# Kernel optimization log

Hardware: AMD Instinct MI355X
Metric: run time of the kernel (lower is better)

The kernel has to match this reference:

```python
import math
import jax, jax.numpy as jnp
import numpy as np

H = 16  # num_heads
B, L, D = 1, 256, 1024


def setup_inputs() -> dict:
    key = jax.random.key(0)
    ks = jax.random.split(key, 12)
    s = 1.0 / math.sqrt(D)  # keep activations O(1)
    inp = {
        "mu": jax.random.normal(ks[0], (B, L, D), jnp.float32),
        "var": jax.random.uniform(ks[1], (B, L, D), jnp.float32) + 0.1,
    }
    names = ["q_mu", "q_var", "k_mu", "k_var", "v_mu", "v_var", "o_mu", "o_var"]
    for i, n in enumerate(names):
        inp["w" + n] = jax.random.normal(ks[2 + i], (D, D), jnp.float32) * s
        inp["b" + n] = jnp.zeros((D,), jnp.float32)
    return inp


def _split_heads(x):
    b, l, d = x.shape
    return x.reshape(b, l, H, d // H).transpose(0, 2, 1, 3)  # [B,H,L,Dh]


def _combine_heads(x):
    b, h, l, dh = x.shape
    return x.transpose(0, 2, 1, 3).reshape(b, l, h * dh)


def reference(mu, var, wq_mu, bq_mu, wq_var, bq_var, wk_mu, bk_mu, wk_var, bk_var,
              wv_mu, bv_mu, wv_var, bv_var, wo_mu, bo_mu, wo_var, bo_var):
    dk = mu.shape[-1] // H
    Qm = _split_heads(mu @ wq_mu + bq_mu)
    Qv = _split_heads(jax.nn.softplus(var @ wq_var + bq_var))
    Km = _split_heads(mu @ wk_mu + bk_mu)
    Kv = _split_heads(jax.nn.softplus(var @ wk_var + bk_var))
    Vm = _split_heads(mu @ wv_mu + bv_mu)
    Vv = _split_heads(jax.nn.softplus(var @ wv_var + bv_var))

    # per-element Gaussian KL, broadcast to [B,H,Lq,Lk,Dh] (as in the original)
    diff = (Qm[:, :, :, None, :] - Km[:, :, None, :, :]) ** 2
    ratio = Qv[:, :, :, None, :] / Kv[:, :, None, :, :]
    kl = diff / (2.0 * Kv[:, :, None, :, :]) + 0.5 * (ratio - jnp.log(ratio) - 1.0)
    scores = -kl.sum(-1) * (1.0 / math.sqrt(dk))  # [B,H,Lq,Lk]
    attn = jax.nn.softmax(scores, axis=-1)

    out_mu = jnp.einsum("bhqk,bhkd->bhqd", attn, Vm)
    out_var = jnp.einsum("bhqk,bhkd->bhqd", attn ** 2, Vv)

    O_mu = _combine_heads(out_mu)
    O_var = _combine_heads(out_var)
    mu_out = O_mu @ wo_mu + bo_mu
    var_out = jax.nn.softplus(O_var @ wo_var + bo_var)
    return mu_out, var_out
```

## Files before the change

kernel.cpp:

```cpp
#include <hip/hip_runtime.h>
#include <math.h>

typedef __bf16 bf16_t;
typedef bf16_t bf16x4 __attribute__((ext_vector_type(4)));
typedef bf16_t bf16x8 __attribute__((ext_vector_type(8)));
typedef float  f32x4  __attribute__((ext_vector_type(4)));

__device__ __forceinline__ float softplus_f(float x) {
    return (x > 20.f) ? x : log1pf(expf(x));
}

__device__ __forceinline__ float fast_rcp(float x) {
#if __has_builtin(__builtin_amdgcn_rcpf)
    return __builtin_amdgcn_rcpf(x);
#else
    return 1.0f / x;
#endif
}

template<bool AF32, int MT>
__device__ __forceinline__ void gemmT_core(const void* Aptr, const float* __restrict__ Wf,
                                           const int m_base, const int n_base,
                                           unsigned char* smem, const int t, f32x4* out) {
    constexpr int NA  = 2 * MT;
    constexpr int SWS = MT * 1152 + 4608;
    constexpr int CRS = MT * 1088;
    __syncthreads();
    bf16_t* stage = (bf16_t*)smem;
    float*  Cr    = (float*)smem;
    const int lane = t & 63, w = t >> 6;
    bf16_t* As = stage + w * SWS;
    bf16_t* Bs = As + MT * 1152;
    const int r8 = lane >> 3, kb = lane & 7;
    const int fr = lane & 15, fq = lane >> 4, fk = fq * 8;
    const int bc = fr;
    const int br16 = fq * 16;

    const float*  Af = (const float*)Aptr  + (size_t)m_base * 1024 + w * 256 + kb * 8;
    const bf16_t* Ab = (const bf16_t*)Aptr + (size_t)m_base * 1024 + w * 256 + kb * 8;
    const float*  Bf = Wf + (size_t)(w * 256 + br16) * 1024 + n_base + bc * 4;

    f32x4 acc[MT][4] = {};
    bf16x8 pa[NA];
    f32x4 paf0[NA], paf1[NA];
    f32x4 pbf[16];

#pragma unroll
    for (int i = 0; i < NA; ++i) {
        if constexpr (AF32) {
            paf0[i] = *(const f32x4*)(Af + (size_t)(i * 8 + r8) * 1024);
            paf1[i] = *(const f32x4*)(Af + (size_t)(i * 8 + r8) * 1024 + 4);
        } else {
            pa[i] = *(const bf16x8*)(Ab + (size_t)(i * 8 + r8) * 1024);
        }
    }
#pragma unroll
    for (int i = 0; i < 16; ++i)
        pbf[i] = *(const f32x4*)(Bf + (size_t)i * 1024);

#pragma unroll
    for (int s = 0; s < 4; ++s) {
#pragma unroll
        for (int i = 0; i < NA; ++i) {
            bf16x8 av;
            if constexpr (AF32) {
#pragma unroll
                for (int e = 0; e < 4; ++e) {
                    av[e]     = (bf16_t)paf0[i][e];
                    av[e + 4] = (bf16_t)paf1[i][e];
                }
            } else {
                av = pa[i];
            }
            *(bf16x8*)&As[(i * 8 + r8) * 72 + kb * 8] = av;
        }
#pragma unroll
        for (int e = 0; e < 4; ++e) {
            bf16x8 lo, hi;
#pragma unroll
            for (int q = 0; q < 8; ++q) {
                lo[q] = (bf16_t)pbf[q][e];
                hi[q] = (bf16_t)pbf[q + 8][e];
            }
            *(bf16x8*)&Bs[(bc * 4 + e) * 72 + br16]     = lo;
            *(bf16x8*)&Bs[(bc * 4 + e) * 72 + br16 + 8] = hi;
        }
        if (s < 3) {
            const int off = (s + 1) * 64;
#pragma unroll
            for (int i = 0; i < NA; ++i) {
                if constexpr (AF32) {
                    paf0[i] = *(const f32x4*)(Af + (size_t)(i * 8 + r8) * 1024 + off);
                    paf1[i] = *(const f32x4*)(Af + (size_t)(i * 8 + r8) * 1024 + off + 4);
                } else {
                    pa[i] = *(const bf16x8*)(Ab + (size_t)(i * 8 + r8) * 1024 + off);
                }
            }
#pragma unroll
            for (int i = 0; i < 16; ++i)
                pbf[i] = *(const f32x4*)(Bf + (size_t)i * 1024 + (size_t)off * 1024);
        }
#pragma unroll
        for (int kh = 0; kh < 2; ++kh) {
            bf16x8 aF[MT], bF[4];
#pragma unroll
            for (int i = 0; i < MT; ++i)
                aF[i] = *(const bf16x8*)&As[(i * 16 + fr) * 72 + kh * 32 + fk];
#pragma unroll
            for (int j = 0; j < 4; ++j)
                bF[j] = *(const bf16x8*)&Bs[(j * 16 + fr) * 72 + kh * 32 + fk];
#pragma unroll
            for (int i = 0; i < MT; ++i)
#pragma unroll
                for (int j = 0; j < 4; ++j)
                    acc[i][j] = __builtin_amdgcn_mfma_f32_16x16x32_bf16(aF[i], bF[j], acc[i][j], 0, 0, 0);
        }
    }

    __syncthreads();
    {
        float* Crw = Cr + w * CRS;
        const int orow = fq * 4;
#pragma unroll
        for (int i = 0; i < MT; ++i)
#pragma unroll
            for (int j = 0; j < 4; ++j)
#pragma unroll
                for (int rr = 0; rr < 4; ++rr)
                    Crw[(i * 16 + orow + rr) * 68 + j * 16 + fr] = acc[i][j][rr];
    }
    __syncthreads();

    const int cc = (t & 15) * 4;
#pragma unroll
    for (int i = 0; i < MT; ++i) {
        const int row = (t >> 4) + i * 16;
        f32x4 s0 = *(const f32x4*)&Cr[0 * CRS + row * 68 + cc];
        f32x4 s1 = *(const f32x4*)&Cr[1 * CRS + row * 68 + cc];
        f32x4 s2 = *(const f32x4*)&Cr[2 * CRS + row * 68 + cc];
        f32x4 s3 = *(const f32x4*)&Cr[3 * CRS + row * 68 + cc];
        out[i] = (s0 + s1) + (s2 + s3);
    }
}

__device__ __forceinline__ void gemmK_dual(const float* __restrict__ mu,
                                           const float* __restrict__ var,
                                           const float* __restrict__ Wkm,
                                           const float* __restrict__ Wkv,
                                           const int m_base, const int n_base,
                                           unsigned char* smem, const int t,
                                           f32x4 okm[2], f32x4 okv[2]) {
    constexpr int SWS = 2 * 1152 + 4608;
    constexpr int CRS = 2 * 1088;
    __syncthreads();
    bf16_t* stage = (bf16_t*)smem;
    float*  Cr    = (float*)smem;
    const int lane = t & 63, w = t >> 6;
    bf16_t* As = stage + w * SWS;
    bf16_t* Bs = As + 2 * 1152;
    const int r8 = lane >> 3, kb = lane & 7;
    const int fr = lane & 15, fq = lane >> 4, fk = fq * 8;
    const int bc = fr;
    const int br16 = fq * 16;

    const float* Asrc = (w < 2) ? mu : var;
    const float* Wsrc = (w < 2) ? Wkm : Wkv;
    const int kbase = (w & 1) * 512;

    const float* Af = Asrc + (size_t)m_base * 1024 + kbase + kb * 8;
    const float* Bf = Wsrc + (size_t)(kbase + br16) * 1024 + n_base + bc * 4;

    f32x4 acc[2][4] = {};
    f32x4 paf0[4], paf1[4];
    f32x4 pbf[16];

#pragma unroll
    for (int i = 0; i < 4; ++i) {
        paf0[i] = *(const f32x4*)(Af + (size_t)(i * 8 + r8) * 1024);
        paf1[i] = *(const f32x4*)(Af + (size_t)(i * 8 + r8) * 1024 + 4);
    }
#pragma unroll
    for (int i = 0; i < 16; ++i)
        pbf[i] = *(const f32x4*)(Bf + (size_t)i * 1024);

#pragma unroll
    for (int s = 0; s < 8; ++s) {
#pragma unroll
        for (int i = 0; i < 4; ++i) {
            bf16x8 av;
#pragma unroll
            for (int e = 0; e < 4; ++e) {
                av[e]     = (bf16_t)paf0[i][e];
                av[e + 4] = (bf16_t)paf1[i][e];
            }
            *(bf16x8*)&As[(i * 8 + r8) * 72 + kb * 8] = av;
        }
#pragma unroll
        for (int e = 0; e < 4; ++e) {
            bf16x8 lo, hi;
#pragma unroll
            for (int q = 0; q < 8; ++q) {
                lo[q] = (bf16_t)pbf[q][e];
                hi[q] = (bf16_t)pbf[q + 8][e];
            }
            *(bf16x8*)&Bs[(bc * 4 + e) * 72 + br16]     = lo;
            *(bf16x8*)&Bs[(bc * 4 + e) * 72 + br16 + 8] = hi;
        }
        if (s < 7) {
            const int off = (s + 1) * 64;
#pragma unroll
            for (int i = 0; i < 4; ++i) {
                paf0[i] = *(const f32x4*)(Af + (size_t)(i * 8 + r8) * 1024 + off);
                paf1[i] = *(const f32x4*)(Af + (size_t)(i * 8 + r8) * 1024 + off + 4);
            }
#pragma unroll
            for (int i = 0; i < 16; ++i)
                pbf[i] = *(const f32x4*)(Bf + (size_t)i * 1024 + (size_t)off * 1024);
        }
#pragma unroll
        for (int kh = 0; kh < 2; ++kh) {
            bf16x8 aF[2], bF[4];
#pragma unroll
            for (int i = 0; i < 2; ++i)
                aF[i] = *(const bf16x8*)&As[(i * 16 + fr) * 72 + kh * 32 + fk];
#pragma unroll
            for (int j = 0; j < 4; ++j)
                bF[j] = *(const bf16x8*)&Bs[(j * 16 + fr) * 72 + kh * 32 + fk];
#pragma unroll
            for (int i = 0; i < 2; ++i)
#pragma unroll
                for (int j = 0; j < 4; ++j)
                    acc[i][j] = __builtin_amdgcn_mfma_f32_16x16x32_bf16(aF[i], bF[j], acc[i][j], 0, 0, 0);
        }
    }

    __syncthreads();
    {
        float* Crw = Cr + w * CRS;
        const int orow = fq * 4;
#pragma unroll
        for (int i = 0; i < 2; ++i)
#pragma unroll
            for (int j = 0; j < 4; ++j)
#pragma unroll
                for (int rr = 0; rr < 4; ++rr)
                    Crw[(i * 16 + orow + rr) * 68 + j * 16 + fr] = acc[i][j][rr];
    }
    __syncthreads();

    const int cc = (t & 15) * 4;
#pragma unroll
    for (int i = 0; i < 2; ++i) {
        const int row = (t >> 4) + i * 16;
        okm[i] = *(const f32x4*)&Cr[0 * CRS + row * 68 + cc]
               + *(const f32x4*)&Cr[1 * CRS + row * 68 + cc];
        okv[i] = *(const f32x4*)&Cr[2 * CRS + row * 68 + cc]
               + *(const f32x4*)&Cr[3 * CRS + row * 68 + cc];
    }
}

#define PROJ_SMEM 55296

struct ProjArgs {
    const float* mu; const float* var;
    const float* W[6];
    const float* bias[6];
    float* Proj;
    bf16_t* Vbm; bf16_t* Vbv;
    bf16_t* Gbf; float* cvec;
};

__global__ __launch_bounds__(256, 2) void proj_kernel(ProjArgs a) {
    __shared__ __align__(16) unsigned char smem[PROJ_SMEM];
    const int t = threadIdx.x;
    const int cc = (t & 15) * 4;
    const int L = blockIdx.x;

    if (L < 128) {
        const int x = L & 7, o = L >> 3;
        const int h  = (o >> 3) * 8 + x;
        const int mb = (o & 7) * 32;
        const int nb = h * 64;
        f32x4 okm[2], okv[2];
        gemmK_dual(a.mu, a.var, a.W[2], a.W[3], mb, nb, smem, t, okm, okv);
        const f32x4 bkm = *(const f32x4*)&a.bias[2][nb + cc];
        const f32x4 bkv = *(const f32x4*)&a.bias[3][nb + cc];
#pragma unroll
        for (int i = 0; i < 2; ++i) {
            const int row = (t >> 4) + i * 16;
            const int katt = mb + row;
            const f32x4 km  = okm[i] + bkm;
            const f32x4 kvr = okv[i] + bkv;
            bf16x4 o1, o2;
            float c = 0.f;
#pragma unroll
            for (int e = 0; e < 4; ++e) {
                const float kv = softplus_f(kvr[e]);
                const float r  = 0.5f * fast_rcp(kv);
                o1[e] = (bf16_t)r;
                o2[e] = (bf16_t)(-2.f * km[e] * r);
                c += km[e] * km[e] * r + 0.5f * __logf(kv);
            }
            bf16_t* grow = a.Gbf + ((size_t)(h * 256 + katt)) * 128;
            *(bf16x4*)&grow[cc]      = o1;
            *(bf16x4*)&grow[64 + cc] = o2;
#pragma unroll
            for (int off = 8; off > 0; off >>= 1)
                c += __shfl_xor(c, off, 16);
            if ((t & 15) == 0)
                a.cvec[h * 256 + katt] = c;
        }
    } else {
        const int Lp = L - 128;
        const int x = Lp & 7, o = Lp >> 3;
        const int panel = (o >> 3) * 8 + x;
        const int mb = (o & 7) * 32;
        const int zp = panel >> 4;
        const int nb = (panel & 15) * 64;
        const int wi = (zp < 2) ? zp : (zp + 2);
        const int sp = (zp == 1) || (zp == 3);
        const void* A = sp ? (const void*)a.var : (const void*)a.mu;
        f32x4 ov[2];
        gemmT_core<true, 2>(A, a.W[wi], mb, nb, smem, t, ov);
        const f32x4 bv = *(const f32x4*)&a.bias[wi][nb + cc];
        if (zp < 2) {
            float* dst = a.Proj + (size_t)zp * 262144;
#pragma unroll
            for (int i = 0; i < 2; ++i) {
                const int row = (t >> 4) + i * 16;
                f32x4 v = ov[i] + bv;
                if (sp) {
                    v[0] = softplus_f(v[0]); v[1] = softplus_f(v[1]);
                    v[2] = softplus_f(v[2]); v[3] = softplus_f(v[3]);
                }
                *(f32x4*)&dst[(size_t)(mb + row) * 1024 + nb + cc] = v;
            }
        } else {
            bf16_t* dst = ((zp == 2) ? a.Vbm : a.Vbv) + (size_t)(nb >> 6) * 16384;
#pragma unroll
            for (int i = 0; i < 2; ++i) {
                const int row = (t >> 4) + i * 16;
                f32x4 v = ov[i] + bv;
                if (sp) {
                    v[0] = softplus_f(v[0]); v[1] = softplus_f(v[1]);
                    v[2] = softplus_f(v[2]); v[3] = softplus_f(v[3]);
                }
                bf16x4 o4;
                o4[0] = (bf16_t)v[0]; o4[1] = (bf16_t)v[1];
                o4[2] = (bf16_t)v[2]; o4[3] = (bf16_t)v[3];
                *(bf16x4*)&dst[(size_t)(mb + row) * 64 + cc] = o4;
            }
        }
    }
}

#define OFF_VM   0
#define OFF_VV   36864
#define OFF_FS   73728
#define OFF_SC   82176
#define OFF_PHI  98816
#define OFF_PLO  107264
#define OFF_P2H  115712
#define OFF_P2L  124160
#define ATTN_SMEM 132608

__global__ __launch_bounds__(512) void attn_v7(const float* __restrict__ Qm,
                                               const float* __restrict__ Qv,
                                               const bf16_t* __restrict__ Gbf,
                                               const float* __restrict__ cvec,
                                               const bf16_t* __restrict__ Vbm,
                                               const bf16_t* __restrict__ Vbv,
                                               bf16_t* __restrict__ Omu,
                                               bf16_t* __restrict__ Ovar) {
    __shared__ __align__(16) unsigned char smem[ATTN_SMEM];
    bf16_t* Vsm = (bf16_t*)(smem + OFF_VM);
    bf16_t* Vsv = (bf16_t*)(smem + OFF_VV);
    float*  Fs  = (float*)(smem + OFF_FS);
    float*  Sc  = (float*)(smem + OFF_SC);
    bf16_t* Phi = (bf16_t*)(smem + OFF_PHI);
    bf16_t* Plo = (bf16_t*)(smem + OFF_PLO);
    bf16_t* P2h = (bf16_t*)(smem + OFF_P2H);
    bf16_t* P2l = (bf16_t*)(smem + OFF_P2L);

    const int L = blockIdx.x;
    const int h  = ((L >> 7) << 3) + (L & 7);
    const int qt = (L >> 3) & 15;

    const int t = threadIdx.x, w = t >> 6, lane = t & 63;
    const int fr = lane & 15, fq = lane >> 4;
    const int n0 = w * 32;

    const bf16_t* gB = Gbf + ((size_t)(h * 256 + n0 + fr)) * 128 + fq * 8;

    bf16x8 bcur[4];
#pragma unroll
    for (int ks = 0; ks < 4; ++ks) bcur[ks] = *(const bf16x8*)(gB + ks * 32);

    if (t < 256) {
        const int r = t >> 4, c = t & 15;
        f32x4 qm = *(const f32x4*)(Qm + (size_t)(qt * 16 + r) * 1024 + h * 64 + c * 4);
        f32x4 qv = *(const f32x4*)(Qv + (size_t)(qt * 16 + r) * 1024 + h * 64 + c * 4);
        *(f32x4*)&Fs[r * 132 + c * 4]      = qm * qm + qv;
        *(f32x4*)&Fs[r * 132 + 64 + c * 4] = qm;
    }
    __syncthreads();

    bf16x8 ahi[4], alo[4];
#pragma unroll
    for (int ks = 0; ks < 4; ++ks) {
        f32x4 f0 = *(const f32x4*)&Fs[fr * 132 + ks * 32 + fq * 8];
        f32x4 f1 = *(const f32x4*)&Fs[fr * 132 + ks * 32 + fq * 8 + 4];
#pragma unroll
        for (int e = 0; e < 4; ++e) {
            bf16_t hb = (bf16_t)f0[e];
            ahi[ks][e] = hb; alo[ks][e] = (bf16_t)(f0[e] - (float)hb);
            bf16_t hb2 = (bf16_t)f1[e];
            ahi[ks][e + 4] = hb2; alo[ks][e + 4] = (bf16_t)(f1[e] - (float)hb2);
        }
    }

    const int tm = t & 255;
    const int vk = tm >> 2, vpart = tm & 3;
    const bf16_t* Vsrc = ((t >= 256) ? Vbv : Vbm) + (size_t)h * 16384;
    bf16_t*      Vdst = (t >= 256) ? Vsv : Vsm;

#pragma unroll
    for (int nt = 0; nt < 2; ++nt) {
        const int ra = vk + (2 * nt) * 64;
        const int rb = vk + (2 * nt + 1) * 64;
        bf16x8 pa0 = *(const bf16x8*)(Vsrc + (size_t)ra * 64 + vpart * 16);
        bf16x8 pa1 = *(const bf16x8*)(Vsrc + (size_t)ra * 64 + vpart * 16 + 8);
        bf16x8 pb0 = *(const bf16x8*)(Vsrc + (size_t)rb * 64 + vpart * 16);
        bf16x8 pb1 = *(const bf16x8*)(Vsrc + (size_t)rb * 64 + vpart * 16 + 8);

        bf16x8 bnxt[4];
        if (nt < 1) {
#pragma unroll
            for (int ks = 0; ks < 4; ++ks)
                bnxt[ks] = *(const bf16x8*)(gB + 2048 + ks * 32);
        }

        f32x4 acc = {0.f, 0.f, 0.f, 0.f};
#pragma unroll
        for (int ks = 0; ks < 4; ++ks) {
            acc = __builtin_amdgcn_mfma_f32_16x16x32_bf16(ahi[ks], bcur[ks], acc, 0, 0, 0);
            acc = __builtin_amdgcn_mfma_f32_16x16x32_bf16(alo[ks], bcur[ks], acc, 0, 0, 0);
        }

        {
            bf16_t* da = Vdst + ra * 72 + vpart * 16;
            bf16_t* db = Vdst + rb * 72 + vpart * 16;
            *(bf16x8*)(da)     = pa0;
            *(bf16x8*)(da + 8) = pa1;
            *(bf16x8*)(db)     = pb0;
            *(bf16x8*)(db + 8) = pb1;
        }

        const float cv = cvec[h * 256 + n0 + nt * 16 + fr];
        f32x4 lg = (acc + cv) * (-0.125f);
#pragma unroll
        for (int reg = 0; reg < 4; ++reg)
            Sc[(fq * 4 + reg) * 260 + n0 + nt * 16 + fr] = lg[reg];

#pragma unroll
        for (int ks = 0; ks < 4; ++ks) bcur[ks] = bnxt[ks];
    }
    __syncthreads();

    const int fw = w * 2;
    f32x4 sr[2];
#pragma unroll
    for (int r = 0; r < 2; ++r)
        sr[r] = *(const f32x4*)&Sc[(fw + r) * 260 + lane * 4];
#pragma unroll
    for (int r = 0; r < 2; ++r) {
        f32x4 s = sr[r];
        float mloc = fmaxf(fmaxf(s[0], s[1]), fmaxf(s[2], s[3]));
#pragma unroll
        for (int off = 32; off > 0; off >>= 1)
            mloc = fmaxf(mloc, __shfl_xor(mloc, off, 64));
        s[0] = __expf(s[0] - mloc); s[1] = __expf(s[1] - mloc);
        s[2] = __expf(s[2] - mloc); s[3] = __expf(s[3] - mloc);
        float sl = (s[0] + s[1]) + (s[2] + s[3]);
#pragma unroll
        for (int off = 32; off > 0; off >>= 1)
            sl += __shfl_xor(sl, off, 64);
        sr[r] = s * fast_rcp(sl);
    }

#pragma unroll
    for (int r = 0; r < 2; ++r) {
        bf16x4 phi, plo, p2hi, p2lo;
#pragma unroll
        for (int e = 0; e < 4; ++e) {
            const float p = sr[r][e];
            const bf16_t hb = (bf16_t)p;
            phi[e] = hb; plo[e] = (bf16_t)(p - (float)hb);
            const float p2 = p * p;
            const bf16_t h2 = (bf16_t)p2;
            p2hi[e] = h2; p2lo[e] = (bf16_t)(p2 - (float)h2);
        }
        const int row = fw + r;
        *(bf16x4*)&Phi[row * 264 + lane * 4] = phi;
        *(bf16x4*)&Plo[row * 264 + lane * 4] = plo;
        *(bf16x4*)&P2h[row * 264 + lane * 4] = p2hi;
        *(bf16x4*)&P2l[row * 264 + lane * 4] = p2lo;
    }
    __syncthreads();

    const int tile = w & 3;
    const int isvar = w >> 2;
    const bf16_t* Pa = isvar ? P2h : Phi;
    const bf16_t* Pb = isvar ? P2l : Plo;
    const bf16_t* Vs = isvar ? Vsv : Vsm;
    f32x4 accp = {0.f, 0.f, 0.f, 0.f};
#pragma unroll
    for (int k0 = 0; k0 < 256; k0 += 32) {
        const int ka = k0 + fq * 8;
        bf16x8 a1 = *(const bf16x8*)&Pa[fr * 264 + ka];
        bf16x8 a2 = *(const bf16x8*)&Pb[fr * 264 + ka];
        bf16x8 bfr;
#pragma unroll
        for (int j = 0; j < 8; ++j)
            bfr[j] = Vs[(ka + j) * 72 + tile * 16 + fr];
        accp = __builtin_amdgcn_mfma_f32_16x16x32_bf16(a1, bfr, accp, 0, 0, 0);
        accp = __builtin_amdgcn_mfma_f32_16x16x32_bf16(a2, bfr, accp, 0, 0, 0);
    }

    bf16_t* Out = isvar ? Ovar : Omu;
#pragma unroll
    for (int reg = 0; reg < 4; ++reg) {
        const int qg = qt * 16 + fq * 4 + reg;
        const size_t ob = (size_t)qg * 1024 + h * 64 + tile * 16 + fr;
        Out[ob] = (bf16_t)accp[reg];
    }
}

struct OutArgs {
    const bf16_t* A[2];
    const float*  W[2];
    const float*  bias[2];
    float*        dst[2];
    int           splus[2];
};

__global__ __launch_bounds__(256, 2) void out_gemm(OutArgs args) {
    __shared__ __align__(16) unsigned char smem[PROJ_SMEM];
    const int t = threadIdx.x;
    const int L = blockIdx.x;
    const int x = L & 7, o = L >> 3;
    const int g = (o >> 3) * 8 + x;
    const int m = o & 7;
    const int z = g >> 4;
    const int n_base = (g & 15) * 64;
    const int m_base = m * 32;

    const bf16_t* __restrict__ A    = args.A[z];
    const float*  __restrict__ W    = args.W[z];
    const float*  __restrict__ bias = args.bias[z];
    float*        __restrict__ dst  = args.dst[z];
    const int sp = args.splus[z];

    f32x4 ov[2];
    gemmT_core<false, 2>(A, W, m_base, n_base, smem, t, ov);

    const int cc = (t & 15) * 4;
    const f32x4 bv = *(const f32x4*)&bias[n_base + cc];
#pragma unroll
    for (int i = 0; i < 2; ++i) {
        const int row = (t >> 4) + i * 16;
        f32x4 v = ov[i] + bv;
        if (sp) {
            v[0] = softplus_f(v[0]); v[1] = softplus_f(v[1]);
            v[2] = softplus_f(v[2]); v[3] = softplus_f(v[3]);
        }
        *(f32x4*)&dst[(size_t)(m_base + row) * 1024 + n_base + cc] = v;
    }
}

extern "C" void kernel_launch(void* const* d_in, const int* in_sizes, int n_in,
                              void* d_out, int out_size, void* d_ws, size_t ws_size,
                              hipStream_t stream) {
    const float* mu  = (const float*)d_in[0];
    const float* var = (const float*)d_in[1];
    uint8_t* ws = (uint8_t*)d_ws;

    float*  Proj = (float*)(ws);
    bf16_t* Vbm  = (bf16_t*)(ws + (2u << 20));
    bf16_t* Vbv  = (bf16_t*)(ws + (2u << 20) + (512u << 10));
    bf16_t* Obm  = (bf16_t*)(ws + (3u << 20));
    bf16_t* Obv  = (bf16_t*)(ws + (3u << 20) + (512u << 10));
    bf16_t* Gbf  = (bf16_t*)(ws + (4u << 20));
    float*  cvec = (float*)(ws + (5u << 20));

    ProjArgs pr;
    pr.mu = mu; pr.var = var;
    for (int i = 0; i < 6; ++i) {
        pr.W[i]    = (const float*)d_in[2 + 2 * i];
        pr.bias[i] = (const float*)d_in[3 + 2 * i];
    }
    pr.Proj = Proj; pr.Vbm = Vbm; pr.Vbv = Vbv; pr.Gbf = Gbf; pr.cvec = cvec;
    proj_kernel<<<dim3(640), 256, 0, stream>>>(pr);

    attn_v7<<<dim3(256), 512, 0, stream>>>(Proj, Proj + 262144, Gbf, cvec,
                                           Vbm, Vbv, Obm, Obv);

    OutArgs g3;
    g3.A[0] = Obm;  g3.W[0] = (const float*)d_in[14];
    g3.bias[0] = (const float*)d_in[15];
    g3.dst[0] = (float*)d_out;             g3.splus[0] = 0;
    g3.A[1] = Obv;  g3.W[1] = (const float*)d_in[16];
    g3.bias[1] = (const float*)d_in[17];
    g3.dst[1] = (float*)d_out + 262144;    g3.splus[1] = 1;
    out_gemm<<<dim3(256), 256, 0, stream>>>(g3);
}
```

Before: 137.1 us.

## Store V transposed in projection and read MFMA B-fragments directly from global

The projection kernel now writes the V mean and variance tensors transposed (head dim major, key index contiguous) using scalar bf16 stores. The attention kernel no longer stages V into shared memory. It loads each 8-element B fragment with one vector global load instead of eight strided LDS reads. This shrinks attention shared memory from about 130KB to about 58KB, which could allow more resident blocks. The cost is uncoalesced scalar transposed writes in the projection kernel and repeated global/L2 reads of V across the 16 query tiles.

```diff
diff --git a/kernel.cpp b/kernel.cpp
--- a/kernel.cpp
+++ b/kernel.cpp
@@ -266,7 +266,7 @@
     const float* W[6];
     const float* bias[6];
     float* Proj;
-    bf16_t* Vbm; bf16_t* Vbv;
+    bf16_t* Vtm; bf16_t* Vtv;
     bf16_t* Gbf; float* cvec;
 };
 
@@ -336,45 +336,41 @@
                 *(f32x4*)&dst[(size_t)(mb + row) * 1024 + nb + cc] = v;
             }
         } else {
-            bf16_t* dst = ((zp == 2) ? a.Vbm : a.Vbv) + (size_t)(nb >> 6) * 16384;
+            bf16_t* dst = ((zp == 2) ? a.Vtm : a.Vtv) + (size_t)(nb >> 6) * 16384;
 #pragma unroll
             for (int i = 0; i < 2; ++i) {
                 const int row = (t >> 4) + i * 16;
+                const int katt = mb + row;
                 f32x4 v = ov[i] + bv;
                 if (sp) {
                     v[0] = softplus_f(v[0]); v[1] = softplus_f(v[1]);
                     v[2] = softplus_f(v[2]); v[3] = softplus_f(v[3]);
                 }
-                bf16x4 o4;
-                o4[0] = (bf16_t)v[0]; o4[1] = (bf16_t)v[1];
-                o4[2] = (bf16_t)v[2]; o4[3] = (bf16_t)v[3];
-                *(bf16x4*)&dst[(size_t)(mb + row) * 64 + cc] = o4;
-            }
-        }
-    }
-}
-
-#define OFF_VM   0
-#define OFF_VV   36864
-#define OFF_FS   73728
-#define OFF_SC   82176
-#define OFF_PHI  98816
-#define OFF_PLO  107264
-#define OFF_P2H  115712
-#define OFF_P2L  124160
-#define ATTN_SMEM 132608
-
-__global__ __launch_bounds__(512) void attn_v7(const float* __restrict__ Qm,
+#pragma unroll
+                for (int e = 0; e < 4; ++e)
+                    dst[(size_t)(cc + e) * 256 + katt] = (bf16_t)v[e];
+            }
+        }
+    }
+}
+
+#define OFF_FS   0
+#define OFF_SC   8448
+#define OFF_PHI  25088
+#define OFF_PLO  33536
+#define OFF_P2H  41984
+#define OFF_P2L  50432
+#define ATTN_SMEM 58880
+
+__global__ __launch_bounds__(512) void attn_v8(const float* __restrict__ Qm,
                                                const float* __restrict__ Qv,
                                                const bf16_t* __restrict__ Gbf,
                                                const float* __restrict__ cvec,
-                                               const bf16_t* __restrict__ Vbm,
-                                               const bf16_t* __restrict__ Vbv,
+                                               const bf16_t* __restrict__ Vtm,
+                                               const bf16_t* __restrict__ Vtv,
                                                bf16_t* __restrict__ Omu,
                                                bf16_t* __restrict__ Ovar) {
     __shared__ __align__(16) unsigned char smem[ATTN_SMEM];
-    bf16_t* Vsm = (bf16_t*)(smem + OFF_VM);
-    bf16_t* Vsv = (bf16_t*)(smem + OFF_VV);
     float*  Fs  = (float*)(smem + OFF_FS);
     float*  Sc  = (float*)(smem + OFF_SC);
     bf16_t* Phi = (bf16_t*)(smem + OFF_PHI);
@@ -419,20 +415,8 @@
         }
     }
 
-    const int tm = t & 255;
-    const int vk = tm >> 2, vpart = tm & 3;
-    const bf16_t* Vsrc = ((t >= 256) ? Vbv : Vbm) + (size_t)h * 16384;
-    bf16_t*      Vdst = (t >= 256) ? Vsv : Vsm;
-
 #pragma unroll
     for (int nt = 0; nt < 2; ++nt) {
-        const int ra = vk + (2 * nt) * 64;
-        const int rb = vk + (2 * nt + 1) * 64;
-        bf16x8 pa0 = *(const bf16x8*)(Vsrc + (size_t)ra * 64 + vpart * 16);
-        bf16x8 pa1 = *(const bf16x8*)(Vsrc + (size_t)ra * 64 + vpart * 16 + 8);
-        bf16x8 pb0 = *(const bf16x8*)(Vsrc + (size_t)rb * 64 + vpart * 16);
-        bf16x8 pb1 = *(const bf16x8*)(Vsrc + (size_t)rb * 64 + vpart * 16 + 8);
-
         bf16x8 bnxt[4];
         if (nt < 1) {
 #pragma unroll
@@ -445,15 +429,6 @@
         for (int ks = 0; ks < 4; ++ks) {
             acc = __builtin_amdgcn_mfma_f32_16x16x32_bf16(ahi[ks], bcur[ks], acc, 0, 0, 0);
             acc = __builtin_amdgcn_mfma_f32_16x16x32_bf16(alo[ks], bcur[ks], acc, 0, 0, 0);
-        }
-
-        {
-            bf16_t* da = Vdst + ra * 72 + vpart * 16;
-            bf16_t* db = Vdst + rb * 72 + vpart * 16;
-            *(bf16x8*)(da)     = pa0;
-            *(bf16x8*)(da + 8) = pa1;
-            *(bf16x8*)(db)     = pb0;
-            *(bf16x8*)(db + 8) = pb1;
         }
 
         const float cv = cvec[h * 256 + n0 + nt * 16 + fr];
@@ -512,17 +487,15 @@
     const int isvar = w >> 2;
     const bf16_t* Pa = isvar ? P2h : Phi;
     const bf16_t* Pb = isvar ? P2l : Plo;
-    const bf16_t* Vs = isvar ? Vsv : Vsm;
+    const bf16_t* Vrow = (isvar ? Vtv : Vtm) + (size_t)h * 16384
+                       + (size_t)(tile * 16 + fr) * 256 + fq * 8;
     f32x4 accp = {0.f, 0.f, 0.f, 0.f};
 #pragma unroll
     for (int k0 = 0; k0 < 256; k0 += 32) {
         const int ka = k0 + fq * 8;
         bf16x8 a1 = *(const bf16x8*)&Pa[fr * 264 + ka];
         bf16x8 a2 = *(const bf16x8*)&Pb[fr * 264 + ka];
-        bf16x8 bfr;
-#pragma unroll
-        for (int j = 0; j < 8; ++j)
-            bfr[j] = Vs[(ka + j) * 72 + tile * 16 + fr];
+        bf16x8 bfr = *(const bf16x8*)(Vrow + k0);
         accp = __builtin_amdgcn_mfma_f32_16x16x32_bf16(a1, bfr, accp, 0, 0, 0);
         accp = __builtin_amdgcn_mfma_f32_16x16x32_bf16(a2, bfr, accp, 0, 0, 0);
     }
@@ -586,8 +559,8 @@
     uint8_t* ws = (uint8_t*)d_ws;
 
     float*  Proj = (float*)(ws);
-    bf16_t* Vbm  = (bf16_t*)(ws + (2u << 20));
-    bf16_t* Vbv  = (bf16_t*)(ws + (2u << 20) + (512u << 10));
+    bf16_t* Vtm  = (bf16_t*)(ws + (2u << 20));
+    bf16_t* Vtv  = (bf16_t*)(ws + (2u << 20) + (512u << 10));
     bf16_t* Obm  = (bf16_t*)(ws + (3u << 20));
     bf16_t* Obv  = (bf16_t*)(ws + (3u << 20) + (512u << 10));
     bf16_t* Gbf  = (bf16_t*)(ws + (4u << 20));
@@ -599,11 +572,11 @@
         pr.W[i]    = (const float*)d_in[2 + 2 * i];
         pr.bias[i] = (const float*)d_in[3 + 2 * i];
     }
-    pr.Proj = Proj; pr.Vbm = Vbm; pr.Vbv = Vbv; pr.Gbf = Gbf; pr.cvec = cvec;
+    pr.Proj = Proj; pr.Vtm = Vtm; pr.Vtv = Vtv; pr.Gbf = Gbf; pr.cvec = cvec;
     proj_kernel<<<dim3(640), 256, 0, stream>>>(pr);
 
-    attn_v7<<<dim3(256), 512, 0, stream>>>(Proj, Proj + 262144, Gbf, cvec,
-                                           Vbm, Vbv, Obm, Obv);
+    attn_v8<<<dim3(256), 512, 0, stream>>>(Proj, Proj + 262144, Gbf, cvec,
+                                           Vtm, Vtv, Obm, Obv);
 
     OutArgs g3;
     g3.A[0] = Obm;  g3.W[0] = (const float*)d_in[14];
```

Result: no change. 137.1 us (+0.0%).
